# Kernel tuning notes

Measured on AMD Instinct MI355X. Metric: run time of the kernel, lower is better.

The kernel has to match this reference:

```python
import jax, jax.numpy as jnp
import numpy as np

B, S, D = 2, 2048, 768
H = 12
HD = D // H


def setup_inputs() -> dict:
    key = jax.random.key(0)
    k1, k2, k3 = jax.random.split(key, 3)
    hidden_states = jax.random.normal(k1, (B, S, D), dtype=jnp.float32)
    Wqkv = jax.random.normal(k2, (D, 3 * D), dtype=jnp.float32) * (1.0 / np.sqrt(D))
    bqkv = jnp.zeros((3 * D,), dtype=jnp.float32)
    Wout = jax.random.normal(k3, (D, D), dtype=jnp.float32) * (1.0 / np.sqrt(D))
    bout = jnp.zeros((D,), dtype=jnp.float32)
    return {"hidden_states": hidden_states, "Wqkv": Wqkv, "bqkv": bqkv,
            "Wout": Wout, "bout": bout}


def reference(hidden_states, Wqkv, bqkv, Wout, bout):
    b, s, d = hidden_states.shape
    h, hd = H, HD
    scale = hd ** -0.5
    qkv = hidden_states @ Wqkv + bqkv                      # [b, s, 3d]
    q, k, v = jnp.split(qkv, 3, axis=-1)
    # [b, h, s, hd]
    q = q.reshape(b, s, h, hd).transpose(0, 2, 1, 3)
    k = k.reshape(b, s, h, hd).transpose(0, 2, 1, 3)
    v = v.reshape(b, s, h, hd).transpose(0, 2, 1, 3)
    scores = jnp.einsum('bhqd,bhkd->bhqk', q, k) * scale   # [b, h, s, s]
    causal = jnp.tril(jnp.ones((s, s), dtype=bool))
    scores = jnp.where(causal, scores, -jnp.inf)
    attn = jax.nn.softmax(scores, axis=-1)
    out = jnp.einsum('bhqk,bhkd->bhqd', attn, v)           # [b, h, s, hd]
    out = out.transpose(0, 2, 1, 3).reshape(b, s, d)
    return out @ Wout + bout
```

## Files before the change

### kernel.cpp

```cpp
#include <hip/hip_runtime.h>
#include <hip/hip_bf16.h>

typedef __attribute__((ext_vector_type(8))) short bf16x8;
typedef __attribute__((ext_vector_type(4))) float f32x4;
typedef __attribute__((ext_vector_type(4))) unsigned int u32x4;

#define NB 2
#define NS 2048
#define ND 768
#define NH 12
#define NHD 64
#define N3D 2304
#define NM (NB * NS)

__device__ __forceinline__ unsigned short f2bf(float x) {
    union { float f; unsigned u; } v; v.f = x;
    unsigned r = v.u + 0x7FFFu + ((v.u >> 16) & 1u);
    return (unsigned short)(r >> 16);
}

__device__ __forceinline__ unsigned cvt_pk_bf16(float lo, float hi) {
    unsigned r;
    asm volatile("v_cvt_pk_bf16_f32 %0, %1, %2" : "=v"(r) : "v"(lo), "v"(hi));
    return r;
}

__global__ __launch_bounds__(256)
void conv_bf16(const float* __restrict__ in, unsigned short* __restrict__ out) {
    const int i = (blockIdx.x * 256 + threadIdx.x) * 4;
    float4 v = *reinterpret_cast<const float4*>(in + i);
    ushort4 o;
    o.x = f2bf(v.x); o.y = f2bf(v.y); o.z = f2bf(v.z); o.w = f2bf(v.w);
    *reinterpret_cast<ushort4*>(out + i) = o;
}

__global__ __launch_bounds__(256)
void transp_conv(const float* __restrict__ in, unsigned short* __restrict__ out,
                 int K, int N) {
    __shared__ float T[32][33];
    const int n0 = blockIdx.x * 32, k0 = blockIdx.y * 32;
    const int r = threadIdx.x >> 3, c4 = (threadIdx.x & 7) * 4;
    float4 v = *reinterpret_cast<const float4*>(&in[(size_t)(k0 + r) * N + n0 + c4]);
    T[r][c4 + 0] = v.x; T[r][c4 + 1] = v.y; T[r][c4 + 2] = v.z; T[r][c4 + 3] = v.w;
    __syncthreads();
    ushort4 o;
    o.x = f2bf(T[c4 + 0][r]); o.y = f2bf(T[c4 + 1][r]);
    o.z = f2bf(T[c4 + 2][r]); o.w = f2bf(T[c4 + 3][r]);
    *reinterpret_cast<ushort4*>(&out[(size_t)(n0 + r) * K + k0 + c4]) = o;
}

__global__ __launch_bounds__(256)
void vtransp(const unsigned short* __restrict__ V, unsigned short* __restrict__ Vt) {
    __shared__ __align__(16) unsigned short T[64][72];
    const int bh = blockIdx.y;
    const int s0 = blockIdx.x * 64;
    const int t = threadIdx.x;
    const unsigned short* src = V + ((size_t)bh * NS + s0) * NHD;
    const int r = t >> 2, cc = (t & 3) * 16;
    *(bf16x8*)&T[r][cc]     = *(const bf16x8*)&src[r * NHD + cc];
    *(bf16x8*)&T[r][cc + 8] = *(const bf16x8*)&src[r * NHD + cc + 8];
    __syncthreads();
    unsigned short* dst = Vt + ((size_t)bh * NHD) * NS + s0;
    const int chunk = t & 7;
#pragma unroll
    for (int h = 0; h < 2; ++h) {
        const int d = (t >> 3) + h * 32;
        bf16x8 v;
#pragma unroll
        for (int e = 0; e < 8; ++e) v[e] = (short)T[chunk * 8 + e][d];
        *(bf16x8*)&dst[(size_t)d * NS + chunk * 8] = v;
    }
}

template<int BM, int BN, int EPI>
__global__ __launch_bounds__(256)
void gemm_k768(const unsigned short* __restrict__ A,
               const unsigned short* __restrict__ Bt,
               const float* __restrict__ bias,
               unsigned short* __restrict__ Qo, unsigned short* __restrict__ Ko,
               unsigned short* __restrict__ Vo, float* __restrict__ Co) {
    __shared__ unsigned short As[2][BM * 64];
    __shared__ unsigned short Bs[2][BN * 64];
    const int t = threadIdx.x;
    const int wv = t >> 6, lane = t & 63;
    const int lr = lane & 15, lg = lane >> 4;
    const int wr = wv >> 1, wc = wv & 1;
    const int m0 = blockIdx.y * BM;
    const int n0 = blockIdx.x * BN;
    constexpr int FM = BM / 32;
    constexpr int FN = BN / 32;

    f32x4 acc[FM][FN];
#pragma unroll
    for (int i = 0; i < FM; ++i)
#pragma unroll
        for (int j = 0; j < FN; ++j) acc[i][j] = (f32x4){0.f, 0.f, 0.f, 0.f};

    const int sr = t >> 3;
    const int sb = t & 7;

#define GSTAGE(buf, k0)                                                          \
    {                                                                            \
        _Pragma("unroll")                                                        \
        for (int jj = 0; jj < BM / 32; ++jj) {                                   \
            const int row = jj * 32 + sr;                                        \
            __builtin_amdgcn_global_load_lds(                                    \
                (const void*)(A + (size_t)(m0 + row) * ND + (k0) + ((sb ^ (row & 7)) * 8)), \
                (void*)(As[buf] + jj * 2048 + wv * 512), 16, 0, 0);              \
        }                                                                        \
        _Pragma("unroll")                                                        \
        for (int jj = 0; jj < BN / 32; ++jj) {                                   \
            const int row = jj * 32 + sr;                                        \
            __builtin_amdgcn_global_load_lds(                                    \
                (const void*)(Bt + (size_t)(n0 + row) * ND + (k0) + ((sb ^ (row & 7)) * 8)), \
                (void*)(Bs[buf] + jj * 2048 + wv * 512), 16, 0, 0);              \
        }                                                                        \
    }

    GSTAGE(0, 0);
    for (int ki = 0; ki < ND / 64; ++ki) {
        __syncthreads();
        if (ki + 1 < ND / 64) GSTAGE((ki + 1) & 1, (ki + 1) * 64);
        const unsigned short* Ac = As[ki & 1];
        const unsigned short* Bc = Bs[ki & 1];
#pragma unroll
        for (int kc = 0; kc < 2; ++kc) {
            bf16x8 af[FM], bfr[FN];
#pragma unroll
            for (int mi = 0; mi < FM; ++mi) {
                const int row = wr * (BM / 2) + mi * 16 + lr;
                af[mi] = *(const bf16x8*)&Ac[row * 64 + (((kc * 4 + lg) ^ (row & 7)) * 8)];
            }
#pragma unroll
            for (int nj = 0; nj < FN; ++nj) {
                const int row = wc * (BN / 2) + nj * 16 + lr;
                bfr[nj] = *(const bf16x8*)&Bc[row * 64 + (((kc * 4 + lg) ^ (row & 7)) * 8)];
            }
#pragma unroll
            for (int mi = 0; mi < FM; ++mi)
#pragma unroll
                for (int nj = 0; nj < FN; ++nj)
                    acc[mi][nj] = __builtin_amdgcn_mfma_f32_16x16x32_bf16(
                        af[mi], bfr[nj], acc[mi][nj], 0, 0, 0);
        }
    }
#undef GSTAGE

    if (EPI == 0) {
        const int sec = n0 / ND;
#pragma unroll
        for (int mi = 0; mi < FM; ++mi) {
#pragma unroll
            for (int nj = 0; nj < FN; ++nj) {
                const int n = n0 + wc * (BN / 2) + nj * 16 + lr;
                const int rem = n - sec * ND;
                const int hh = rem >> 6, dd = rem & 63;
                const float b = bias[n];
#pragma unroll
                for (int r = 0; r < 4; ++r) {
                    const int m = m0 + wr * (BM / 2) + mi * 16 + lg * 4 + r;
                    const int bb = m >> 11, ss = m & (NS - 1);
                    const int bhh = bb * NH + hh;
                    const float v = acc[mi][nj][r] + b;
                    if (sec == 0)
                        Qo[((size_t)bhh * NS + ss) * NHD + dd] = f2bf(v * 0.18033688011112042f);
                    else if (sec == 1)
                        Ko[((size_t)bhh * NS + ss) * NHD + dd] = f2bf(v);
                    else
                        Vo[((size_t)bhh * NS + ss) * NHD + dd] = f2bf(v);
                }
            }
        }
    } else {
#pragma unroll
        for (int mi = 0; mi < FM; ++mi)
#pragma unroll
            for (int nj = 0; nj < FN; ++nj) {
                const int n = n0 + wc * (BN / 2) + nj * 16 + lr;
                const float b = bias[n];
#pragma unroll
                for (int r = 0; r < 4; ++r) {
                    const int m = m0 + wr * (BM / 2) + mi * 16 + lg * 4 + r;
                    Co[(size_t)m * ND + n] = acc[mi][nj][r] + b;
                }
            }
    }
}

__global__ __launch_bounds__(256)
void attn_mfma(const unsigned short* __restrict__ Qg,
               const unsigned short* __restrict__ Kg,
               const unsigned short* __restrict__ Vtg,
               unsigned short* __restrict__ AO) {
    __shared__ unsigned short Ks[2][128 * 64];
    __shared__ unsigned short Vs[2][64 * 128];
    const int n = blockIdx.x;
    const int x = n & 7, ii = n >> 3;
    const int bh = ((ii >> 5) << 3) + x;
    const int qt = (31 - (ii & 31) + 11 * (ii >> 5)) & 31;
    const int t = threadIdx.x;
    const int w = t >> 6, lane = t & 63;
    const int lr = lane & 15, lg = lane >> 4;
    const int lgp = lg & 1;
    const int qrow = qt * 64 + w * 16 + lr;
    const size_t bhoff = (size_t)bh * (NS * NHD);

    const unsigned short* Qp = Qg + bhoff + (size_t)qrow * NHD;
    const bf16x8 qB0 = *(const bf16x8*)(Qp + lg * 8);
    const bf16x8 qB1 = *(const bf16x8*)(Qp + 32 + lg * 8);

    float m_run = -1e30f, l_part = 0.f;
    f32x4 of[4];
#pragma unroll
    for (int f = 0; f < 4; ++f) of[f] = (f32x4){0.f, 0.f, 0.f, 0.f};

    const unsigned short* Kb = Kg + bhoff;
    const unsigned short* Vb = Vtg + bhoff;
    const int ksrow = lane >> 3, ksblk = lane & 7;
    const int vsrow = lane >> 4, vsblk = lane & 15;
    const int ntiles = (qt + 2) >> 1;
    const int bswz = ((lg & 1) << 1) | (lg >> 1);

#define STAGE(buf, kv0)                                                           \
    {                                                                             \
        _Pragma("unroll")                                                         \
        for (int h = 0; h < 4; ++h) {                                             \
            const int rr = w * 32 + h * 8 + ksrow;                                \
            __builtin_amdgcn_global_load_lds(                                     \
                (const void*)(Kb + (size_t)((kv0) + rr) * NHD + ((ksblk ^ (rr & 7)) * 8)),  \
                (void*)(Ks[buf] + (w * 32 + h * 8) * 64), 16, 0, 0);              \
            const int vr = w * 16 + h * 4 + vsrow;                                \
            __builtin_amdgcn_global_load_lds(                                     \
                (const void*)(Vb + (size_t)vr * NS + (kv0) + ((vsblk ^ (vr & 7)) * 8)),     \
                (void*)(Vs[buf] + (w * 16 + h * 4) * 128), 16, 0, 0);             \
        }                                                                         \
    }

    STAGE(0, 0);
    for (int kt = 0; kt < ntiles; ++kt) {
        __syncthreads();
        if (kt + 1 < ntiles) STAGE((kt + 1) & 1, (kt + 1) * 128);
        const unsigned short* Kc = Ks[kt & 1];
        const unsigned short* Vc = Vs[kt & 1];
        const int kv0 = kt * 128;

        f32x4 sf[8];
#pragma unroll
        for (int f = 0; f < 8; ++f) sf[f] = (f32x4){0.f, 0.f, 0.f, 0.f};
        __builtin_amdgcn_s_setprio(1);
#pragma unroll
        for (int f = 0; f < 8; ++f) {
            const int krow = f * 16 + lr;
            const bf16x8 a0 = *(const bf16x8*)&Kc[krow * 64 + ((lg ^ (krow & 7)) * 8)];
            const bf16x8 a1 = *(const bf16x8*)&Kc[krow * 64 + (((4 + lg) ^ (krow & 7)) * 8)];
            sf[f] = __builtin_amdgcn_mfma_f32_16x16x32_bf16(a0, qB0, sf[f], 0, 0, 0);
            sf[f] = __builtin_amdgcn_mfma_f32_16x16x32_bf16(a1, qB1, sf[f], 0, 0, 0);
        }
        __builtin_amdgcn_s_setprio(0);

        if (kt == ntiles - 1) {
            const int thr = qrow - kv0;
#pragma unroll
            for (int f = 0; f < 8; ++f)
#pragma unroll
                for (int r = 0; r < 4; ++r)
                    if (f * 16 + lg * 4 + r > thr) sf[f][r] = -1e30f;
        }

        float tm = -1e30f;
#pragma unroll
        for (int f = 0; f < 8; ++f)
            tm = fmaxf(tm, fmaxf(fmaxf(sf[f][0], sf[f][1]), fmaxf(sf[f][2], sf[f][3])));
        tm = fmaxf(tm, __shfl_xor(tm, 16));
        tm = fmaxf(tm, __shfl_xor(tm, 32));
        if (!__all(tm <= m_run)) {
            const float nm = fmaxf(m_run, tm);
            const float corr = exp2f(m_run - nm);
            m_run = nm;
            l_part *= corr;
#pragma unroll
            for (int f = 0; f < 4; ++f)
#pragma unroll
                for (int r = 0; r < 4; ++r) of[f][r] *= corr;
        }
#pragma unroll
        for (int f = 0; f < 8; ++f)
#pragma unroll
            for (int r = 0; r < 4; ++r) {
                sf[f][r] = exp2f(sf[f][r] - m_run);
                l_part += sf[f][r];
            }

        bf16x8 pb[4];
#pragma unroll
        for (int c = 0; c < 4; ++c) {
            const unsigned A0 = cvt_pk_bf16(sf[2 * c][0], sf[2 * c][1]);
            const unsigned A1 = cvt_pk_bf16(sf[2 * c][2], sf[2 * c][3]);
            const unsigned B0 = cvt_pk_bf16(sf[2 * c + 1][0], sf[2 * c + 1][1]);
            const unsigned B1 = cvt_pk_bf16(sf[2 * c + 1][2], sf[2 * c + 1][3]);
            const unsigned s0 = lgp ? A0 : B0;
            const unsigned s1 = lgp ? A1 : B1;
            const unsigned r0 = (unsigned)__shfl_xor((int)s0, 16);
            const unsigned r1 = (unsigned)__shfl_xor((int)s1, 16);
            const unsigned o0 = lgp ? B0 : A0;
            const unsigned o1 = lgp ? B1 : A1;
            u32x4 wvv;
            wvv[0] = lgp ? r0 : o0;
            wvv[1] = lgp ? r1 : o1;
            wvv[2] = lgp ? o0 : r0;
            wvv[3] = lgp ? o1 : r1;
            pb[c] = __builtin_bit_cast(bf16x8, wvv);
        }

        __builtin_amdgcn_s_setprio(1);
#pragma unroll
        for (int fA = 0; fA < 4; ++fA) {
            const int drow = fA * 16 + lr;
#pragma unroll
            for (int c = 0; c < 4; ++c) {
                const int blk = 4 * c + bswz;
                const bf16x8 va = *(const bf16x8*)&Vc[drow * 128 + ((blk ^ (drow & 7)) * 8)];
                of[fA] = __builtin_amdgcn_mfma_f32_16x16x32_bf16(va, pb[c], of[fA], 0, 0, 0);
            }
        }
        __builtin_amdgcn_s_setprio(0);
    }
#undef STAGE

    l_part += __shfl_xor(l_part, 16);
    l_part += __shfl_xor(l_part, 32);
    const float inv = 1.f / l_part;
    const int bb = bh / NH, hh = bh - bb * NH;
    unsigned short* op = AO + ((size_t)(bb * NS + qrow)) * ND + hh * NHD;
#pragma unroll
    for (int fA = 0; fA < 4; ++fA) {
        ushort4 o4;
        o4.x = f2bf(of[fA][0] * inv);
        o4.y = f2bf(of[fA][1] * inv);
        o4.z = f2bf(of[fA][2] * inv);
        o4.w = f2bf(of[fA][3] * inv);
        *reinterpret_cast<ushort4*>(op + fA * 16 + lg * 4) = o4;
    }
}

extern "C" void kernel_launch(void* const* d_in, const int* in_sizes, int n_in,
                              void* d_out, int out_size, void* d_ws, size_t ws_size,
                              hipStream_t stream) {
    const float* hs   = (const float*)d_in[0];
    const float* Wqkv = (const float*)d_in[1];
    const float* bqkv = (const float*)d_in[2];
    const float* Wout = (const float*)d_in[3];
    const float* bout = (const float*)d_in[4];
    float* out = (float*)d_out;

    char* wp = (char*)d_ws;
    unsigned short* hsb = (unsigned short*)wp; wp += (size_t)NM * ND * 2;
    unsigned short* W1t = (unsigned short*)wp; wp += (size_t)N3D * ND * 2;
    unsigned short* W2t = (unsigned short*)wp; wp += (size_t)ND * ND * 2;
    const size_t per = (size_t)NB * NH * NS * NHD;
    unsigned short* Qb  = (unsigned short*)wp; wp += per * 2;
    unsigned short* Kb  = (unsigned short*)wp; wp += per * 2;
    unsigned short* Vtb = (unsigned short*)wp; wp += per * 2;
    unsigned short* AOb = (unsigned short*)wp; wp += per * 2;

    conv_bf16<<<(NM * ND) / 1024, 256, 0, stream>>>(hs, hsb);
    transp_conv<<<dim3(N3D / 32, ND / 32), 256, 0, stream>>>(Wqkv, W1t, ND, N3D);
    transp_conv<<<dim3(ND / 32, ND / 32), 256, 0, stream>>>(Wout, W2t, ND, ND);

    gemm_k768<128, 128, 0><<<dim3(N3D / 128, NM / 128), 256, 0, stream>>>(
        hsb, W1t, bqkv, Qb, Kb, AOb, nullptr);

    vtransp<<<dim3(NS / 64, NB * NH), 256, 0, stream>>>(AOb, Vtb);

    attn_mfma<<<dim3(NS / 64 * NB * NH), 256, 0, stream>>>(Qb, Kb, Vtb, AOb);

    gemm_k768<64, 64, 1><<<dim3(ND / 64, NM / 64), 256, 0, stream>>>(
        AOb, W2t, bout, nullptr, nullptr, nullptr, out);
}
```

Before: 192.6 us.

## Merge prep kernels, single-buffer GEMM staging, shrink attention KV tile

Folds the activation conversion and both weight transpose-converts into one launch, removing two kernel launches. The GEMM loses its double-buffered global-to-LDS prefetch and now loads, syncs, then computes each k-step, which halves its shared memory but exposes load latency. The attention kernel moves from 128-wide to 64-wide KV tiles. That halves its LDS footprint and trims causal-mask waste on the diagonal, at the cost of more loop iterations and more softmax rescales.

```diff
diff --git a/kernel.cpp b/kernel.cpp
--- a/kernel.cpp
+++ b/kernel.cpp
@@ -25,20 +25,11 @@
     return r;
 }
 
-__global__ __launch_bounds__(256)
-void conv_bf16(const float* __restrict__ in, unsigned short* __restrict__ out) {
-    const int i = (blockIdx.x * 256 + threadIdx.x) * 4;
-    float4 v = *reinterpret_cast<const float4*>(in + i);
-    ushort4 o;
-    o.x = f2bf(v.x); o.y = f2bf(v.y); o.z = f2bf(v.z); o.w = f2bf(v.w);
-    *reinterpret_cast<ushort4*>(out + i) = o;
-}
-
-__global__ __launch_bounds__(256)
-void transp_conv(const float* __restrict__ in, unsigned short* __restrict__ out,
-                 int K, int N) {
-    __shared__ float T[32][33];
-    const int n0 = blockIdx.x * 32, k0 = blockIdx.y * 32;
+__device__ __forceinline__ void transp_tile(const float* __restrict__ in,
+                                            unsigned short* __restrict__ out,
+                                            int K, int N, int nt, int kt,
+                                            float (*T)[33]) {
+    const int n0 = nt * 32, k0 = kt * 32;
     const int r = threadIdx.x >> 3, c4 = (threadIdx.x & 7) * 4;
     float4 v = *reinterpret_cast<const float4*>(&in[(size_t)(k0 + r) * N + n0 + c4]);
     T[r][c4 + 0] = v.x; T[r][c4 + 1] = v.y; T[r][c4 + 2] = v.z; T[r][c4 + 3] = v.w;
@@ -47,6 +38,27 @@
     o.x = f2bf(T[c4 + 0][r]); o.y = f2bf(T[c4 + 1][r]);
     o.z = f2bf(T[c4 + 2][r]); o.w = f2bf(T[c4 + 3][r]);
     *reinterpret_cast<ushort4*>(&out[(size_t)(n0 + r) * K + k0 + c4]) = o;
+}
+
+__global__ __launch_bounds__(256)
+void prep(const float* __restrict__ hs, unsigned short* __restrict__ hsb,
+          const float* __restrict__ Wqkv, unsigned short* __restrict__ W1t,
+          const float* __restrict__ Wout, unsigned short* __restrict__ W2t) {
+    __shared__ float T[32][33];
+    const int bid = blockIdx.x;
+    if (bid < 3072) {
+        const int i = (bid * 256 + threadIdx.x) * 4;
+        float4 v = *reinterpret_cast<const float4*>(hs + i);
+        ushort4 o;
+        o.x = f2bf(v.x); o.y = f2bf(v.y); o.z = f2bf(v.z); o.w = f2bf(v.w);
+        *reinterpret_cast<ushort4*>(hsb + i) = o;
+    } else if (bid < 3072 + 1728) {
+        const int idx = bid - 3072;
+        transp_tile(Wqkv, W1t, ND, N3D, idx % 72, idx / 72, T);
+    } else {
+        const int idx = bid - 4800;
+        transp_tile(Wout, W2t, ND, ND, idx % 24, idx / 24, T);
+    }
 }
 
 __global__ __launch_bounds__(256)
@@ -79,8 +91,8 @@
                const float* __restrict__ bias,
                unsigned short* __restrict__ Qo, unsigned short* __restrict__ Ko,
                unsigned short* __restrict__ Vo, float* __restrict__ Co) {
-    __shared__ unsigned short As[2][BM * 64];
-    __shared__ unsigned short Bs[2][BN * 64];
+    __shared__ unsigned short As[BM * 64];
+    __shared__ unsigned short Bs[BN * 64];
     const int t = threadIdx.x;
     const int wv = t >> 6, lane = t & 63;
     const int lr = lane & 15, lg = lane >> 4;
@@ -99,42 +111,36 @@
     const int sr = t >> 3;
     const int sb = t & 7;
 
-#define GSTAGE(buf, k0)                                                          \
-    {                                                                            \
-        _Pragma("unroll")                                                        \
-        for (int jj = 0; jj < BM / 32; ++jj) {                                   \
-            const int row = jj * 32 + sr;                                        \
-            __builtin_amdgcn_global_load_lds(                                    \
-                (const void*)(A + (size_t)(m0 + row) * ND + (k0) + ((sb ^ (row & 7)) * 8)), \
-                (void*)(As[buf] + jj * 2048 + wv * 512), 16, 0, 0);              \
-        }                                                                        \
-        _Pragma("unroll")                                                        \
-        for (int jj = 0; jj < BN / 32; ++jj) {                                   \
-            const int row = jj * 32 + sr;                                        \
-            __builtin_amdgcn_global_load_lds(                                    \
-                (const void*)(Bt + (size_t)(n0 + row) * ND + (k0) + ((sb ^ (row & 7)) * 8)), \
-                (void*)(Bs[buf] + jj * 2048 + wv * 512), 16, 0, 0);              \
-        }                                                                        \
-    }
-
-    GSTAGE(0, 0);
     for (int ki = 0; ki < ND / 64; ++ki) {
+        const int k0 = ki * 64;
         __syncthreads();
-        if (ki + 1 < ND / 64) GSTAGE((ki + 1) & 1, (ki + 1) * 64);
-        const unsigned short* Ac = As[ki & 1];
-        const unsigned short* Bc = Bs[ki & 1];
+#pragma unroll
+        for (int jj = 0; jj < BM / 32; ++jj) {
+            const int row = jj * 32 + sr;
+            __builtin_amdgcn_global_load_lds(
+                (const void*)(A + (size_t)(m0 + row) * ND + k0 + ((sb ^ (row & 7)) * 8)),
+                (void*)(As + jj * 2048 + wv * 512), 16, 0, 0);
+        }
+#pragma unroll
+        for (int jj = 0; jj < BN / 32; ++jj) {
+            const int row = jj * 32 + sr;
+            __builtin_amdgcn_global_load_lds(
+                (const void*)(Bt + (size_t)(n0 + row) * ND + k0 + ((sb ^ (row & 7)) * 8)),
+                (void*)(Bs + jj * 2048 + wv * 512), 16, 0, 0);
+        }
+        __syncthreads();
 #pragma unroll
         for (int kc = 0; kc < 2; ++kc) {
             bf16x8 af[FM], bfr[FN];
 #pragma unroll
             for (int mi = 0; mi < FM; ++mi) {
                 const int row = wr * (BM / 2) + mi * 16 + lr;
-                af[mi] = *(const bf16x8*)&Ac[row * 64 + (((kc * 4 + lg) ^ (row & 7)) * 8)];
+                af[mi] = *(const bf16x8*)&As[row * 64 + (((kc * 4 + lg) ^ (row & 7)) * 8)];
             }
 #pragma unroll
             for (int nj = 0; nj < FN; ++nj) {
                 const int row = wc * (BN / 2) + nj * 16 + lr;
-                bfr[nj] = *(const bf16x8*)&Bc[row * 64 + (((kc * 4 + lg) ^ (row & 7)) * 8)];
+                bfr[nj] = *(const bf16x8*)&Bs[row * 64 + (((kc * 4 + lg) ^ (row & 7)) * 8)];
             }
 #pragma unroll
             for (int mi = 0; mi < FM; ++mi)
@@ -144,7 +150,6 @@
                         af[mi], bfr[nj], acc[mi][nj], 0, 0, 0);
         }
     }
-#undef GSTAGE
 
     if (EPI == 0) {
         const int sec = n0 / ND;
@@ -192,8 +197,8 @@
                const unsigned short* __restrict__ Kg,
                const unsigned short* __restrict__ Vtg,
                unsigned short* __restrict__ AO) {
-    __shared__ unsigned short Ks[2][128 * 64];
-    __shared__ unsigned short Vs[2][64 * 128];
+    __shared__ unsigned short Ks[2][64 * 64];
+    __shared__ unsigned short Vs[2][64 * 64];
     const int n = blockIdx.x;
     const int x = n & 7, ii = n >> 3;
     const int bh = ((ii >> 5) << 3) + x;
@@ -216,40 +221,38 @@
 
     const unsigned short* Kb = Kg + bhoff;
     const unsigned short* Vb = Vtg + bhoff;
-    const int ksrow = lane >> 3, ksblk = lane & 7;
-    const int vsrow = lane >> 4, vsblk = lane & 15;
-    const int ntiles = (qt + 2) >> 1;
+    const int srow = lane >> 3, sblk = lane & 7;
+    const int ntiles = qt + 1;
     const int bswz = ((lg & 1) << 1) | (lg >> 1);
 
 #define STAGE(buf, kv0)                                                           \
     {                                                                             \
         _Pragma("unroll")                                                         \
-        for (int h = 0; h < 4; ++h) {                                             \
-            const int rr = w * 32 + h * 8 + ksrow;                                \
+        for (int h = 0; h < 2; ++h) {                                             \
+            const int rr = w * 16 + h * 8 + srow;                                 \
             __builtin_amdgcn_global_load_lds(                                     \
-                (const void*)(Kb + (size_t)((kv0) + rr) * NHD + ((ksblk ^ (rr & 7)) * 8)),  \
-                (void*)(Ks[buf] + (w * 32 + h * 8) * 64), 16, 0, 0);              \
-            const int vr = w * 16 + h * 4 + vsrow;                                \
+                (const void*)(Kb + (size_t)((kv0) + rr) * NHD + ((sblk ^ (rr & 7)) * 8)),  \
+                (void*)(Ks[buf] + (w * 16 + h * 8) * 64), 16, 0, 0);              \
             __builtin_amdgcn_global_load_lds(                                     \
-                (const void*)(Vb + (size_t)vr * NS + (kv0) + ((vsblk ^ (vr & 7)) * 8)),     \
-                (void*)(Vs[buf] + (w * 16 + h * 4) * 128), 16, 0, 0);             \
+                (const void*)(Vb + (size_t)rr * NS + (kv0) + ((sblk ^ (rr & 7)) * 8)),     \
+                (void*)(Vs[buf] + (w * 16 + h * 8) * 64), 16, 0, 0);              \
         }                                                                         \
     }
 
     STAGE(0, 0);
     for (int kt = 0; kt < ntiles; ++kt) {
         __syncthreads();
-        if (kt + 1 < ntiles) STAGE((kt + 1) & 1, (kt + 1) * 128);
+        if (kt + 1 < ntiles) STAGE((kt + 1) & 1, (kt + 1) * 64);
         const unsigned short* Kc = Ks[kt & 1];
         const unsigned short* Vc = Vs[kt & 1];
-        const int kv0 = kt * 128;
-
-        f32x4 sf[8];
-#pragma unroll
-        for (int f = 0; f < 8; ++f) sf[f] = (f32x4){0.f, 0.f, 0.f, 0.f};
+        const int kv0 = kt * 64;
+
+        f32x4 sf[4];
+#pragma unroll
+        for (int f = 0; f < 4; ++f) sf[f] = (f32x4){0.f, 0.f, 0.f, 0.f};
         __builtin_amdgcn_s_setprio(1);
 #pragma unroll
-        for (int f = 0; f < 8; ++f) {
+        for (int f = 0; f < 4; ++f) {
             const int krow = f * 16 + lr;
             const bf16x8 a0 = *(const bf16x8*)&Kc[krow * 64 + ((lg ^ (krow & 7)) * 8)];
             const bf16x8 a1 = *(const bf16x8*)&Kc[krow * 64 + (((4 + lg) ^ (krow & 7)) * 8)];
@@ -261,7 +264,7 @@
         if (kt == ntiles - 1) {
             const int thr = qrow - kv0;
 #pragma unroll
-            for (int f = 0; f < 8; ++f)
+            for (int f = 0; f < 4; ++f)
 #pragma unroll
                 for (int r = 0; r < 4; ++r)
                     if (f * 16 + lg * 4 + r > thr) sf[f][r] = -1e30f;
@@ -269,7 +272,7 @@
 
         float tm = -1e30f;
 #pragma unroll
-        for (int f = 0; f < 8; ++f)
+        for (int f = 0; f < 4; ++f)
             tm = fmaxf(tm, fmaxf(fmaxf(sf[f][0], sf[f][1]), fmaxf(sf[f][2], sf[f][3])));
         tm = fmaxf(tm, __shfl_xor(tm, 16));
         tm = fmaxf(tm, __shfl_xor(tm, 32));
@@ -284,16 +287,16 @@
                 for (int r = 0; r < 4; ++r) of[f][r] *= corr;
         }
 #pragma unroll
-        for (int f = 0; f < 8; ++f)
+        for (int f = 0; f < 4; ++f)
 #pragma unroll
             for (int r = 0; r < 4; ++r) {
                 sf[f][r] = exp2f(sf[f][r] - m_run);
                 l_part += sf[f][r];
             }
 
-        bf16x8 pb[4];
-#pragma unroll
-        for (int c = 0; c < 4; ++c) {
+        bf16x8 pb[2];
+#pragma unroll
+        for (int c = 0; c < 2; ++c) {
             const unsigned A0 = cvt_pk_bf16(sf[2 * c][0], sf[2 * c][1]);
             const unsigned A1 = cvt_pk_bf16(sf[2 * c][2], sf[2 * c][3]);
             const unsigned B0 = cvt_pk_bf16(sf[2 * c + 1][0], sf[2 * c + 1][1]);
@@ -317,9 +320,9 @@
         for (int fA = 0; fA < 4; ++fA) {
             const int drow = fA * 16 + lr;
 #pragma unroll
-            for (int c = 0; c < 4; ++c) {
+            for (int c = 0; c < 2; ++c) {
                 const int blk = 4 * c + bswz;
-                const bf16x8 va = *(const bf16x8*)&Vc[drow * 128 + ((blk ^ (drow & 7)) * 8)];
+                const bf16x8 va = *(const bf16x8*)&Vc[drow * 64 + ((blk ^ (drow & 7)) * 8)];
                 of[fA] = __builtin_amdgcn_mfma_f32_16x16x32_bf16(va, pb[c], of[fA], 0, 0, 0);
             }
         }
@@ -363,9 +366,7 @@
     unsigned short* Vtb = (unsigned short*)wp; wp += per * 2;
     unsigned short* AOb = (unsigned short*)wp; wp += per * 2;
 
-    conv_bf16<<<(NM * ND) / 1024, 256, 0, stream>>>(hs, hsb);
-    transp_conv<<<dim3(N3D / 32, ND / 32), 256, 0, stream>>>(Wqkv, W1t, ND, N3D);
-    transp_conv<<<dim3(ND / 32, ND / 32), 256, 0, stream>>>(Wout, W2t, ND, ND);
+    prep<<<3072 + 1728 + 576, 256, 0, stream>>>(hs, hsb, Wqkv, W1t, Wout, W2t);
 
     gemm_k768<128, 128, 0><<<dim3(N3D / 128, NM / 128), 256, 0, stream>>>(
         hsb, W1t, bqkv, Qb, Kb, AOb, nullptr);
```

After: 184.5 us. -4.2%, faster.
